# Kernel tuning notes

Measured on AMD Instinct MI355X. Metric: run time of the kernel, lower is better.

Reference implementation:

```python
import jax, jax.numpy as jnp
import numpy as np

N_HEADS = 16

def setup_inputs() -> dict:
    key = jax.random.key(0)
    k1, k2, k3 = jax.random.split(key, 3)
    B, T, C = 2, 2048, 1024
    x = jax.random.normal(k1, (B, T, C), dtype=jnp.float32)
    w_attn = jax.random.normal(k2, (3 * C, C), dtype=jnp.float32) * (C ** -0.5)
    b_attn = jnp.zeros((3 * C,), dtype=jnp.float32)
    w_proj = jax.random.normal(k3, (C, C), dtype=jnp.float32) * (C ** -0.5)
    b_proj = jnp.zeros((C,), dtype=jnp.float32)
    return {"x": x, "w_attn": w_attn, "b_attn": b_attn, "w_proj": w_proj, "b_proj": b_proj}

def reference(x, w_attn, b_attn, w_proj, b_proj):
    B, T, C = x.shape
    H = N_HEADS
    Dh = C // H
    qkv = x @ w_attn.T + b_attn                      # [B,T,3C]
    q, k, v = jnp.split(qkv, 3, axis=-1)             # each [B,T,C]
    q = q.reshape(B, T, H, Dh).transpose(0, 2, 1, 3)  # [B,H,T,Dh]
    k = k.reshape(B, T, H, Dh).transpose(0, 2, 1, 3)
    v = v.reshape(B, T, H, Dh).transpose(0, 2, 1, 3)
    scores = jnp.einsum('bhqd,bhkd->bhqk', q, k) * (Dh ** -0.5)  # [B,H,T,T]
    causal = jnp.tril(jnp.ones((T, T), dtype=bool))
    scores = jnp.where(causal, scores, jnp.float32(-jnp.inf))
    probs = jax.nn.softmax(scores, axis=-1)
    out = jnp.einsum('bhqk,bhkd->bhqd', probs, v)    # [B,H,T,Dh]
    out = out.transpose(0, 2, 1, 3).reshape(B, T, C)
    out = out @ w_proj.T + b_proj
    return out
```

## Files before the change

kernel.cpp:

```cpp
#include <hip/hip_runtime.h>
#include <math.h>

#define GB 2
#define GT_SEQ 2048
#define GC 1024
#define GH 16
#define GDH 64
#define GM (GB * GT_SEQ)

typedef __attribute__((ext_vector_type(8))) short bf16x8;
typedef __attribute__((ext_vector_type(8))) unsigned short u16x8;
typedef __attribute__((ext_vector_type(4))) unsigned short u16x4;
typedef __attribute__((ext_vector_type(4))) float f32x4;
typedef unsigned int u32;

#define QSCALE 0.18033688f

__device__ __forceinline__ unsigned short f2bf(float f) {
    unsigned int u = __float_as_uint(f);
    u += 0x7FFFu + ((u >> 16) & 1u);
    return (unsigned short)(u >> 16);
}
__device__ __forceinline__ float bf2f(unsigned short u) {
    return __uint_as_float(((unsigned int)u) << 16);
}
__device__ __forceinline__ float hw_exp2(float x) {
    return __builtin_amdgcn_exp2f(x);
}
__device__ __forceinline__ u32 pack2bf(float lo, float hi) {
    return ((u32)f2bf(hi) << 16) | (u32)f2bf(lo);
}

#define GLOAD_LDS16(g, l) __builtin_amdgcn_global_load_lds( \
    (const __attribute__((address_space(1))) void*)(g),      \
    (__attribute__((address_space(3))) void*)(l), 16, 0, 0)

__device__ __forceinline__ bf16x8 frag_ld(const char* base, int r, int kch) {
    return *reinterpret_cast<const bf16x8*>(base + r * 128 + ((kch ^ (r & 7)) << 4));
}

__global__ __launch_bounds__(256) void cast3_f32_bf16(
    const float* __restrict__ a, unsigned short* __restrict__ oa, int na,
    const float* __restrict__ b, unsigned short* __restrict__ ob, int nb,
    const float* __restrict__ c, unsigned short* __restrict__ oc)
{
    const int i = (blockIdx.x * 256 + threadIdx.x) * 4;
    const float* src; unsigned short* dst; int off;
    if (i < na)            { src = a; dst = oa; off = i; }
    else if (i < na + nb)  { src = b; dst = ob; off = i - na; }
    else                   { src = c; dst = oc; off = i - na - nb; }
    const float4 v = *reinterpret_cast<const float4*>(&src[off]);
    ushort4 o;
    o.x = f2bf(v.x); o.y = f2bf(v.y); o.z = f2bf(v.z); o.w = f2bf(v.w);
    *reinterpret_cast<ushort4*>(&dst[off]) = o;
}

__global__ __launch_bounds__(256) void gemm_mfma_bt(
    const unsigned short* __restrict__ A,
    const unsigned short* __restrict__ B,
    const float* __restrict__ bias,
    float* __restrict__ Cf,
    unsigned short* __restrict__ Cb,
    int M, int N, int K)
{
    __shared__ char As[128 * 128];
    __shared__ char Bs[128 * 128];

    const int tid  = threadIdx.x;
    const int lane = tid & 63;
    const int w    = tid >> 6;
    const int wm   = w >> 1;
    const int wn   = w & 1;
    const int m0 = blockIdx.y * 128;
    const int n0 = blockIdx.x * 128;

    f32x4 acc[4][4];
#pragma unroll
    for (int i = 0; i < 4; ++i)
#pragma unroll
        for (int j = 0; j < 4; ++j) acc[i][j] = (f32x4){0.f, 0.f, 0.f, 0.f};

    const int wbase = (tid & ~63);

    for (int k0 = 0; k0 < K; k0 += 64) {
        const char* Ag = (const char*)(A + (size_t)m0 * K + k0);
        const char* Bg = (const char*)(B + (size_t)n0 * K + k0);
#pragma unroll
        for (int i = 0; i < 4; ++i) {
            const int c = i * 256 + tid;
            const int row = c >> 3, cin = c & 7;
            const size_t goff = (size_t)row * (K * 2) + (size_t)((cin ^ (row & 7)) << 4);
            GLOAD_LDS16(Ag + goff, As + (i * 256 + wbase) * 16);
            GLOAD_LDS16(Bg + goff, Bs + (i * 256 + wbase) * 16);
        }
        __syncthreads();

#pragma unroll
        for (int ks = 0; ks < 2; ++ks) {
            const int kch = ks * 4 + (lane >> 4);
            bf16x8 a[4], b[4];
#pragma unroll
            for (int mi = 0; mi < 4; ++mi)
                a[mi] = frag_ld(As, wm * 64 + mi * 16 + (lane & 15), kch);
#pragma unroll
            for (int ni = 0; ni < 4; ++ni)
                b[ni] = frag_ld(Bs, wn * 64 + ni * 16 + (lane & 15), kch);
#pragma unroll
            for (int mi = 0; mi < 4; ++mi)
#pragma unroll
                for (int ni = 0; ni < 4; ++ni)
                    acc[mi][ni] = __builtin_amdgcn_mfma_f32_16x16x32_bf16(
                        a[mi], b[ni], acc[mi][ni], 0, 0, 0);
        }
        __syncthreads();
    }

    const int lc  = lane & 15;
    const int lr4 = (lane >> 4) * 4;
#pragma unroll
    for (int ni = 0; ni < 4; ++ni) {
        const int gcol = n0 + wn * 64 + ni * 16 + lc;
        const float bv = bias[gcol];
#pragma unroll
        for (int mi = 0; mi < 4; ++mi) {
            const int grow0 = m0 + wm * 64 + mi * 16 + lr4;
#pragma unroll
            for (int j = 0; j < 4; ++j) {
                const float v = acc[mi][ni][j] + bv;
                if (Cb) Cb[(size_t)(grow0 + j) * N + gcol] = f2bf(v);
                else    Cf[(size_t)(grow0 + j) * N + gcol] = v;
            }
        }
    }
}

__global__ __launch_bounds__(256) void transpose_v(
    const unsigned short* __restrict__ qkvb, unsigned short* __restrict__ Vt)
{
    __shared__ unsigned short vt[64][72];
    const int tid = threadIdx.x;
    const int t0  = blockIdx.x * 64;
    const int bh  = blockIdx.y;
    const int b = bh >> 4, h = bh & 15;
    const unsigned short* src = qkvb + (size_t)(b * GT_SEQ) * (3 * GC) + 2 * GC + h * GDH;
    unsigned short* dstb = Vt + (size_t)bh * GDH * GT_SEQ;

#pragma unroll
    for (int i = 0; i < 2; ++i) {
        const int c = i * 256 + tid;
        const int tr = c >> 3, ch = c & 7;
        *reinterpret_cast<u16x8*>(&vt[tr][ch * 8]) =
            *reinterpret_cast<const u16x8*>(src + (size_t)(t0 + tr) * (3 * GC) + ch * 8);
    }
    __syncthreads();
#pragma unroll
    for (int i = 0; i < 2; ++i) {
        const int c = i * 256 + tid;
        const int d = c >> 3, ch = c & 7;
        u16x8 o;
#pragma unroll
        for (int e = 0; e < 8; ++e) o[e] = vt[ch * 8 + e][d];
        *reinterpret_cast<u16x8*>(dstb + (size_t)d * GT_SEQ + t0 + ch * 8) = o;
    }
}

__global__ __launch_bounds__(256) void flash_attn_mfma8(
    const unsigned short* __restrict__ qkvb,
    const unsigned short* __restrict__ Vt,
    unsigned short* __restrict__ O)
{
    __shared__ __align__(16) char Ks[2][64 * 128];
    __shared__ __align__(16) char Vs[2][64 * 128];

    const int tid  = threadIdx.x;
    const int lane = tid & 63;
    const int w    = tid >> 6;
    const int l15  = lane & 15;
    const int l4   = lane >> 4;
    const int bid  = blockIdx.x;
    const int xcd  = bid & 7;
    const int rest = bid >> 3;
    const int bh   = xcd * 4 + (rest & 3);
    const int qb   = 15 - (rest >> 2);
    const int b    = bh >> 4, h = bh & 15;
    const int q0w  = qb * 128 + w * 32;

    const unsigned short* hQ = qkvb + (size_t)(b * GT_SEQ) * (3 * GC) + h * GDH;
    const char* hKc = (const char*)(qkvb + (size_t)(b * GT_SEQ) * (3 * GC) + GC + h * GDH);
    const char* hVc = (const char*)(Vt + (size_t)bh * GDH * GT_SEQ);

    bf16x8 qf[2][2];
#pragma unroll
    for (int mi = 0; mi < 2; ++mi)
#pragma unroll
        for (int s = 0; s < 2; ++s) {
            bf16x8 v = *reinterpret_cast<const bf16x8*>(
                hQ + (size_t)(q0w + mi * 16 + l15) * (3 * GC) + s * 32 + l4 * 8);
#pragma unroll
            for (int e = 0; e < 8; ++e)
                v[e] = (short)f2bf(bf2f((unsigned short)v[e]) * QSCALE);
            qf[mi][s] = v;
        }

    f32x4 acc_o[2][4];
    float l_part[2];
    float m_r[2];
#pragma unroll
    for (int mi = 0; mi < 2; ++mi) {
        l_part[mi] = 0.f;
        m_r[mi] = -1e30f;
#pragma unroll
        for (int nd = 0; nd < 4; ++nd) acc_o[mi][nd] = (f32x4){0.f, 0.f, 0.f, 0.f};
    }

    const int nt = qb * 2 + 2;
    const int wbase16 = (tid & ~63) * 16;

    auto STAGE = [&](int bb, int t) {
        const int k0 = t * 64;
#pragma unroll
        for (int i = 0; i < 2; ++i) {
            const int c = i * 256 + tid;
            const int row = c >> 3, cin = c & 7;
            GLOAD_LDS16(hKc + (size_t)(k0 + row) * (3 * GC * 2) + ((cin ^ (row & 7)) << 4),
                        Ks[bb] + i * 4096 + wbase16);
            GLOAD_LDS16(hVc + (size_t)row * 4096 + (size_t)k0 * 2 + ((cin ^ (row & 7)) << 4),
                        Vs[bb] + i * 4096 + wbase16);
        }
    };

    STAGE(0, 0);
    __syncthreads();

    for (int t = 0; t < nt; ++t) {
        if (t + 1 < nt) STAGE((t + 1) & 1, t + 1);

        const int k0 = t * 64;
        const char* Kb = Ks[t & 1];
        const char* Vb = Vs[t & 1];

        if (k0 <= q0w + 31) {
            f32x4 s_acc[2][4];
#pragma unroll
            for (int mi = 0; mi < 2; ++mi)
#pragma unroll
                for (int ni = 0; ni < 4; ++ni) s_acc[mi][ni] = (f32x4){0.f, 0.f, 0.f, 0.f};
#pragma unroll
            for (int s = 0; s < 2; ++s) {
                bf16x8 kf[4];
#pragma unroll
                for (int ni = 0; ni < 4; ++ni)
                    kf[ni] = frag_ld(Kb, ni * 16 + l15, s * 4 + l4);
#pragma unroll
                for (int ni = 0; ni < 4; ++ni)
#pragma unroll
                    for (int mi = 0; mi < 2; ++mi)
                        s_acc[mi][ni] = __builtin_amdgcn_mfma_f32_16x16x32_bf16(
                            kf[ni], qf[mi][s], s_acc[mi][ni], 0, 0, 0);
            }

            if (k0 + 63 > q0w) {
#pragma unroll
                for (int mi = 0; mi < 2; ++mi)
#pragma unroll
                    for (int ni = 0; ni < 4; ++ni)
#pragma unroll
                        for (int j = 0; j < 4; ++j)
                            if (k0 + ni * 16 + l4 * 4 + j > q0w + mi * 16 + l15)
                                s_acc[mi][ni][j] = -1e30f;
            }

            float rp[2];
            int ok = 1;
#pragma unroll
            for (int mi = 0; mi < 2; ++mi) {
                float r = fmaxf(fmaxf(s_acc[mi][0][0], s_acc[mi][0][1]),
                                fmaxf(s_acc[mi][0][2], s_acc[mi][0][3]));
#pragma unroll
                for (int ni = 1; ni < 4; ++ni)
                    r = fmaxf(r, fmaxf(fmaxf(s_acc[mi][ni][0], s_acc[mi][ni][1]),
                                       fmaxf(s_acc[mi][ni][2], s_acc[mi][ni][3])));
                rp[mi] = r;
                ok &= (r <= m_r[mi] + 8.f) ? 1 : 0;
            }
            if (!__all(ok)) {
#pragma unroll
                for (int mi = 0; mi < 2; ++mi) {
                    float r = rp[mi];
                    r = fmaxf(r, __shfl_xor(r, 16));
                    r = fmaxf(r, __shfl_xor(r, 32));
                    const float mnew = fmaxf(m_r[mi], r);
                    const float corr = hw_exp2(m_r[mi] - mnew);
                    m_r[mi] = mnew;
                    l_part[mi] *= corr;
#pragma unroll
                    for (int nd = 0; nd < 4; ++nd) acc_o[mi][nd] *= corr;
                }
            }

#pragma unroll
            for (int s = 0; s < 2; ++s) {
                union { u32 w4[4]; bf16x8 v; } pw[2];
#pragma unroll
                for (int mi = 0; mi < 2; ++mi) {
                    f32x4 pa, pb;
#pragma unroll
                    for (int j = 0; j < 4; ++j) {
                        pa[j] = hw_exp2(s_acc[mi][2 * s + 0][j] - m_r[mi]);
                        pb[j] = hw_exp2(s_acc[mi][2 * s + 1][j] - m_r[mi]);
                    }
                    l_part[mi] += (pa[0] + pa[1]) + (pa[2] + pa[3])
                                + (pb[0] + pb[1]) + (pb[2] + pb[3]);
                    pw[mi].w4[0] = pack2bf(pa[0], pa[1]);
                    pw[mi].w4[1] = pack2bf(pa[2], pa[3]);
                    pw[mi].w4[2] = pack2bf(pb[0], pb[1]);
                    pw[mi].w4[3] = pack2bf(pb[2], pb[3]);
                }
                const int ch0 = s * 4 + (l4 >> 1);
                const int sub = (l4 & 1) * 8;
#pragma unroll
                for (int nd = 0; nd < 4; ++nd) {
                    const int d  = nd * 16 + l15;
                    const char* vrow = Vb + d * 128;
                    union { u16x4 h2[2]; bf16x8 v; } vbs;
                    vbs.h2[0] = *reinterpret_cast<const u16x4*>(
                        vrow + ((ch0 ^ (d & 7)) << 4) + sub);
                    vbs.h2[1] = *reinterpret_cast<const u16x4*>(
                        vrow + (((ch0 + 2) ^ (d & 7)) << 4) + sub);
#pragma unroll
                    for (int mi = 0; mi < 2; ++mi)
                        acc_o[mi][nd] = __builtin_amdgcn_mfma_f32_16x16x32_bf16(
                            vbs.v, pw[mi].v, acc_o[mi][nd], 0, 0, 0);
                }
            }
        }

        __syncthreads();
    }

#pragma unroll
    for (int mi = 0; mi < 2; ++mi) {
        float lp = l_part[mi];
        lp += __shfl_xor(lp, 16);
        lp += __shfl_xor(lp, 32);
        const float inv = 1.f / lp;
        const int q = q0w + mi * 16 + l15;
        const size_t rbase = (size_t)(b * GT_SEQ + q) * GC + h * GDH;
#pragma unroll
        for (int nd = 0; nd < 4; ++nd) {
            ushort4 ov;
            ov.x = f2bf(acc_o[mi][nd][0] * inv);
            ov.y = f2bf(acc_o[mi][nd][1] * inv);
            ov.z = f2bf(acc_o[mi][nd][2] * inv);
            ov.w = f2bf(acc_o[mi][nd][3] * inv);
            *reinterpret_cast<ushort4*>(&O[rbase + nd * 16 + l4 * 4]) = ov;
        }
    }
}

extern "C" void kernel_launch(void* const* d_in, const int* in_sizes, int n_in,
                              void* d_out, int out_size, void* d_ws, size_t ws_size,
                              hipStream_t stream) {
    (void)in_sizes; (void)n_in; (void)out_size; (void)ws_size;
    const float* x      = (const float*)d_in[0];
    const float* w_attn = (const float*)d_in[1];
    const float* b_attn = (const float*)d_in[2];
    const float* w_proj = (const float*)d_in[3];
    const float* b_proj = (const float*)d_in[4];
    float* out = (float*)d_out;

    unsigned short* xb   = (unsigned short*)d_ws;
    unsigned short* wab  = xb   + (size_t)GM * GC;
    unsigned short* wpb  = wab  + (size_t)3 * GC * GC;
    unsigned short* qkvb = wpb  + (size_t)GC * GC;
    unsigned short* Vt   = qkvb + (size_t)GM * 3 * GC;
    unsigned short* aob  = xb;

    cast3_f32_bf16<<<dim3(8192), dim3(256), 0, stream>>>(
        x, xb, GM * GC, w_attn, wab, 3 * GC * GC, w_proj, wpb);

    gemm_mfma_bt<<<dim3(3 * GC / 128, GM / 128), dim3(256), 0, stream>>>(
        xb, wab, b_attn, nullptr, qkvb, GM, 3 * GC, GC);

    transpose_v<<<dim3(GT_SEQ / 64, GB * GH), dim3(256), 0, stream>>>(qkvb, Vt);

    flash_attn_mfma8<<<dim3(512), dim3(256), 0, stream>>>(qkvb, Vt, aob);

    gemm_mfma_bt<<<dim3(GC / 128, GM / 128), dim3(256), 0, stream>>>(
        aob, wpb, b_proj, out, nullptr, GM, GC, GC);
}
```

Measured before the change: 121.9 us.

## Halve flash-attention query tile to 64 rows, doubling grid to 1024 blocks

The attention kernel now gives each block 64 query rows, with each wave handling 16 rows instead of 32. The grid doubles to 1024 blocks and the per-wave register state (accumulators, Q fragments, softmax stats) is halved. This aims to improve load balance across the causal triangle and raise occupancy. In exchange, each K/V tile staged in LDS is reused by half as many query rows, so global and LDS traffic per unit of work roughly doubles.

After: 118.3 us. 1.03x faster.

```diff
diff --git a/kernel.cpp b/kernel.cpp
--- a/kernel.cpp
+++ b/kernel.cpp
@@ -164,7 +164,7 @@
     }
 }
 
-__global__ __launch_bounds__(256) void flash_attn_mfma8(
+__global__ __launch_bounds__(256) void flash_attn_mfma9(
     const unsigned short* __restrict__ qkvb,
     const unsigned short* __restrict__ Vt,
     unsigned short* __restrict__ O)
@@ -181,39 +181,32 @@
     const int xcd  = bid & 7;
     const int rest = bid >> 3;
     const int bh   = xcd * 4 + (rest & 3);
-    const int qb   = 15 - (rest >> 2);
+    const int qb   = 31 - (rest >> 2);
     const int b    = bh >> 4, h = bh & 15;
-    const int q0w  = qb * 128 + w * 32;
+    const int q0w  = qb * 64 + w * 16;
 
     const unsigned short* hQ = qkvb + (size_t)(b * GT_SEQ) * (3 * GC) + h * GDH;
     const char* hKc = (const char*)(qkvb + (size_t)(b * GT_SEQ) * (3 * GC) + GC + h * GDH);
     const char* hVc = (const char*)(Vt + (size_t)bh * GDH * GT_SEQ);
 
-    bf16x8 qf[2][2];
-#pragma unroll
-    for (int mi = 0; mi < 2; ++mi)
-#pragma unroll
-        for (int s = 0; s < 2; ++s) {
-            bf16x8 v = *reinterpret_cast<const bf16x8*>(
-                hQ + (size_t)(q0w + mi * 16 + l15) * (3 * GC) + s * 32 + l4 * 8);
-#pragma unroll
-            for (int e = 0; e < 8; ++e)
-                v[e] = (short)f2bf(bf2f((unsigned short)v[e]) * QSCALE);
-            qf[mi][s] = v;
-        }
-
-    f32x4 acc_o[2][4];
-    float l_part[2];
-    float m_r[2];
-#pragma unroll
-    for (int mi = 0; mi < 2; ++mi) {
-        l_part[mi] = 0.f;
-        m_r[mi] = -1e30f;
-#pragma unroll
-        for (int nd = 0; nd < 4; ++nd) acc_o[mi][nd] = (f32x4){0.f, 0.f, 0.f, 0.f};
-    }
-
-    const int nt = qb * 2 + 2;
+    bf16x8 qf[2];
+#pragma unroll
+    for (int s = 0; s < 2; ++s) {
+        bf16x8 v = *reinterpret_cast<const bf16x8*>(
+            hQ + (size_t)(q0w + l15) * (3 * GC) + s * 32 + l4 * 8);
+#pragma unroll
+        for (int e = 0; e < 8; ++e)
+            v[e] = (short)f2bf(bf2f((unsigned short)v[e]) * QSCALE);
+        qf[s] = v;
+    }
+
+    f32x4 acc_o[4];
+    float l_part = 0.f;
+    float m_r = -1e30f;
+#pragma unroll
+    for (int nd = 0; nd < 4; ++nd) acc_o[nd] = (f32x4){0.f, 0.f, 0.f, 0.f};
+
+    const int nt = qb + 1;
     const int wbase16 = (tid & ~63) * 16;
 
     auto STAGE = [&](int bb, int t) {
@@ -239,12 +232,10 @@
         const char* Kb = Ks[t & 1];
         const char* Vb = Vs[t & 1];
 
-        if (k0 <= q0w + 31) {
-            f32x4 s_acc[2][4];
-#pragma unroll
-            for (int mi = 0; mi < 2; ++mi)
-#pragma unroll
-                for (int ni = 0; ni < 4; ++ni) s_acc[mi][ni] = (f32x4){0.f, 0.f, 0.f, 0.f};
+        if (k0 <= q0w + 15) {
+            f32x4 s_acc[4];
+#pragma unroll
+            for (int ni = 0; ni < 4; ++ni) s_acc[ni] = (f32x4){0.f, 0.f, 0.f, 0.f};
 #pragma unroll
             for (int s = 0; s < 2; ++s) {
                 bf16x8 kf[4];
@@ -253,68 +244,53 @@
                     kf[ni] = frag_ld(Kb, ni * 16 + l15, s * 4 + l4);
 #pragma unroll
                 for (int ni = 0; ni < 4; ++ni)
-#pragma unroll
-                    for (int mi = 0; mi < 2; ++mi)
-                        s_acc[mi][ni] = __builtin_amdgcn_mfma_f32_16x16x32_bf16(
-                            kf[ni], qf[mi][s], s_acc[mi][ni], 0, 0, 0);
+                    s_acc[ni] = __builtin_amdgcn_mfma_f32_16x16x32_bf16(
+                        kf[ni], qf[s], s_acc[ni], 0, 0, 0);
             }
 
             if (k0 + 63 > q0w) {
 #pragma unroll
-                for (int mi = 0; mi < 2; ++mi)
-#pragma unroll
-                    for (int ni = 0; ni < 4; ++ni)
-#pragma unroll
-                        for (int j = 0; j < 4; ++j)
-                            if (k0 + ni * 16 + l4 * 4 + j > q0w + mi * 16 + l15)
-                                s_acc[mi][ni][j] = -1e30f;
-            }
-
-            float rp[2];
-            int ok = 1;
-#pragma unroll
-            for (int mi = 0; mi < 2; ++mi) {
-                float r = fmaxf(fmaxf(s_acc[mi][0][0], s_acc[mi][0][1]),
-                                fmaxf(s_acc[mi][0][2], s_acc[mi][0][3]));
-#pragma unroll
-                for (int ni = 1; ni < 4; ++ni)
-                    r = fmaxf(r, fmaxf(fmaxf(s_acc[mi][ni][0], s_acc[mi][ni][1]),
-                                       fmaxf(s_acc[mi][ni][2], s_acc[mi][ni][3])));
-                rp[mi] = r;
-                ok &= (r <= m_r[mi] + 8.f) ? 1 : 0;
-            }
+                for (int ni = 0; ni < 4; ++ni)
+#pragma unroll
+                    for (int j = 0; j < 4; ++j)
+                        if (k0 + ni * 16 + l4 * 4 + j > q0w + l15)
+                            s_acc[ni][j] = -1e30f;
+            }
+
+            float r = fmaxf(fmaxf(s_acc[0][0], s_acc[0][1]),
+                            fmaxf(s_acc[0][2], s_acc[0][3]));
+#pragma unroll
+            for (int ni = 1; ni < 4; ++ni)
+                r = fmaxf(r, fmaxf(fmaxf(s_acc[ni][0], s_acc[ni][1]),
+                                   fmaxf(s_acc[ni][2], s_acc[ni][3])));
+            const int ok = (r <= m_r + 8.f) ? 1 : 0;
             if (!__all(ok)) {
-#pragma unroll
-                for (int mi = 0; mi < 2; ++mi) {
-                    float r = rp[mi];
-                    r = fmaxf(r, __shfl_xor(r, 16));
-                    r = fmaxf(r, __shfl_xor(r, 32));
-                    const float mnew = fmaxf(m_r[mi], r);
-                    const float corr = hw_exp2(m_r[mi] - mnew);
-                    m_r[mi] = mnew;
-                    l_part[mi] *= corr;
-#pragma unroll
-                    for (int nd = 0; nd < 4; ++nd) acc_o[mi][nd] *= corr;
-                }
+                r = fmaxf(r, __shfl_xor(r, 16));
+                r = fmaxf(r, __shfl_xor(r, 32));
+                const float mnew = fmaxf(m_r, r);
+                const float corr = hw_exp2(m_r - mnew);
+                m_r = mnew;
+                l_part *= corr;
+#pragma unroll
+                for (int nd = 0; nd < 4; ++nd) acc_o[nd] *= corr;
             }
 
 #pragma unroll
             for (int s = 0; s < 2; ++s) {
-                union { u32 w4[4]; bf16x8 v; } pw[2];
-#pragma unroll
-                for (int mi = 0; mi < 2; ++mi) {
+                union { u32 w4[4]; bf16x8 v; } pw;
+                {
                     f32x4 pa, pb;
 #pragma unroll
                     for (int j = 0; j < 4; ++j) {
-                        pa[j] = hw_exp2(s_acc[mi][2 * s + 0][j] - m_r[mi]);
-                        pb[j] = hw_exp2(s_acc[mi][2 * s + 1][j] - m_r[mi]);
+                        pa[j] = hw_exp2(s_acc[2 * s + 0][j] - m_r);
+                        pb[j] = hw_exp2(s_acc[2 * s + 1][j] - m_r);
                     }
-                    l_part[mi] += (pa[0] + pa[1]) + (pa[2] + pa[3])
-                                + (pb[0] + pb[1]) + (pb[2] + pb[3]);
-                    pw[mi].w4[0] = pack2bf(pa[0], pa[1]);
-                    pw[mi].w4[1] = pack2bf(pa[2], pa[3]);
-                    pw[mi].w4[2] = pack2bf(pb[0], pb[1]);
-                    pw[mi].w4[3] = pack2bf(pb[2], pb[3]);
+                    l_part += (pa[0] + pa[1]) + (pa[2] + pa[3])
+                            + (pb[0] + pb[1]) + (pb[2] + pb[3]);
+                    pw.w4[0] = pack2bf(pa[0], pa[1]);
+                    pw.w4[1] = pack2bf(pa[2], pa[3]);
+                    pw.w4[2] = pack2bf(pb[0], pb[1]);
+                    pw.w4[3] = pack2bf(pb[2], pb[3]);
                 }
                 const int ch0 = s * 4 + (l4 >> 1);
                 const int sub = (l4 & 1) * 8;
@@ -327,10 +303,8 @@
                         vrow + ((ch0 ^ (d & 7)) << 4) + sub);
                     vbs.h2[1] = *reinterpret_cast<const u16x4*>(
                         vrow + (((ch0 + 2) ^ (d & 7)) << 4) + sub);
-#pragma unroll
-                    for (int mi = 0; mi < 2; ++mi)
-                        acc_o[mi][nd] = __builtin_amdgcn_mfma_f32_16x16x32_bf16(
-                            vbs.v, pw[mi].v, acc_o[mi][nd], 0, 0, 0);
+                    acc_o[nd] = __builtin_amdgcn_mfma_f32_16x16x32_bf16(
+                        vbs.v, pw.v, acc_o[nd], 0, 0, 0);
                 }
             }
         }
@@ -338,21 +312,20 @@
         __syncthreads();
     }
 
-#pragma unroll
-    for (int mi = 0; mi < 2; ++mi) {
-        float lp = l_part[mi];
+    {
+        float lp = l_part;
         lp += __shfl_xor(lp, 16);
         lp += __shfl_xor(lp, 32);
         const float inv = 1.f / lp;
-        const int q = q0w + mi * 16 + l15;
+        const int q = q0w + l15;
         const size_t rbase = (size_t)(b * GT_SEQ + q) * GC + h * GDH;
 #pragma unroll
         for (int nd = 0; nd < 4; ++nd) {
             ushort4 ov;
-            ov.x = f2bf(acc_o[mi][nd][0] * inv);
-            ov.y = f2bf(acc_o[mi][nd][1] * inv);
-            ov.z = f2bf(acc_o[mi][nd][2] * inv);
-            ov.w = f2bf(acc_o[mi][nd][3] * inv);
+            ov.x = f2bf(acc_o[nd][0] * inv);
+            ov.y = f2bf(acc_o[nd][1] * inv);
+            ov.z = f2bf(acc_o[nd][2] * inv);
+            ov.w = f2bf(acc_o[nd][3] * inv);
             *reinterpret_cast<ushort4*>(&O[rbase + nd * 16 + l4 * 4]) = ov;
         }
     }
@@ -384,7 +357,7 @@
 
     transpose_v<<<dim3(GT_SEQ / 64, GB * GH), dim3(256), 0, stream>>>(qkvb, Vt);
 
-    flash_attn_mfma8<<<dim3(512), dim3(256), 0, stream>>>(qkvb, Vt, aob);
+    flash_attn_mfma9<<<dim3(1024), dim3(256), 0, stream>>>(qkvb, Vt, aob);
 
     gemm_mfma_bt<<<dim3(GC / 128, GM / 128), dim3(256), 0, stream>>>(
         aob, wpb, b_proj, out, nullptr, GM, GC, GC);
```
